# Optimization experiments

Hardware: AMD Instinct MI355X
Metric: run time of the kernel (lower is better)

Reference implementation:

```python
import jax, jax.numpy as jnp
import numpy as np

B, P, E, F = 65536, 16, 32, 64  # batch, n_patches, n_edges, feature_dim


def setup_inputs() -> dict:
    key = jax.random.key(0)
    k1, k2 = jax.random.split(key, 2)
    node_sections = jax.random.normal(k1, (B, P, F), dtype=jnp.float32)
    incidence = (jax.random.normal(k2, (E, P), dtype=jnp.float32) * 0.1)
    # torch init: each sheaf map = eye(feature_dim) * 0.1, stacked -> [E, F, F]
    sheaf_maps = jnp.tile((jnp.eye(F, dtype=jnp.float32) * 0.1)[None], (E, 1, 1))
    damping = jnp.asarray(0.1, dtype=jnp.float32)
    return {"node_sections": node_sections, "incidence": incidence,
            "sheaf_maps": sheaf_maps, "damping": damping}


def reference(node_sections, incidence, sheaf_maps, damping):
    # Coboundary: weighted[b,e,:] = sum_p incidence[e,p] * sections[b,p,:];
    # then per-edge matmul with sheaf_maps[e].
    weighted = jnp.einsum('ep,bpf->bef', incidence, node_sections)
    coboundary = jnp.einsum('bef,efg->beg', weighted, sheaf_maps)
    # Laplacian diffusion: delta^T delta [P,P] applied over patch dim.
    dTd = jnp.einsum('ep,eq->pq', incidence, incidence)
    diffused = node_sections - damping * jnp.einsum('pq,bqf->bpf', dTd, node_sections)
    # H1 energy proxy: per-edge L2 norm, averaged over edges -> [B]
    h1_norm = jnp.linalg.norm(coboundary, axis=-1).mean(axis=-1)
    return diffused, h1_norm
```

## Files before the change

### kernel.cpp

```cpp
#include <hip/hip_runtime.h>
#include <hip/hip_bf16.h>

typedef __attribute__((ext_vector_type(8))) short short8;
typedef __attribute__((ext_vector_type(4))) float floatx4;

#define NB 65536
#define STS 18
#define WES 68
#define WBS 1092

static __device__ __forceinline__ ushort f2bf(float x) {
  union { float f; unsigned u; } v; v.f = x;
  unsigned r = v.u + 0x7FFFu + ((v.u >> 16) & 1u);
  return (ushort)(r >> 16);
}

__global__ void sheaf_prep(const float* __restrict__ inc,
                           const float* __restrict__ M,
                           const float* __restrict__ damp,
                           ushort* __restrict__ Mt,
                           ushort* __restrict__ L) {
  const int bid = blockIdx.x, tid = threadIdx.x;
  if (bid < 32) {
    const float* Me = M + (bid << 12);
    ushort* Mte = Mt + (bid << 12);
    for (int i = tid; i < 4096; i += 256) {
      int g = i >> 6, f = i & 63;
      Mte[(g << 6) + f] = f2bf(Me[(f << 6) + g]);
    }
  } else {
    for (int i = tid; i < 1024; i += 256) {
      int e = i >> 5, col = i & 31;
      L[(e << 5) + col] = (col < 16) ? f2bf(inc[(e << 4) + col]) : (ushort)0;
    }
    float d = damp[0];
    int p = tid >> 4, q = tid & 15;
    float s = 0.f;
    for (int e = 0; e < 32; ++e)
      s += inc[(e << 4) + p] * inc[(e << 4) + q];
    float a = ((p == q) ? 1.f : 0.f) - d * s;
    L[((32 + p) << 5) + q] = f2bf(a);
    L[((32 + p) << 5) + 16 + q] = (ushort)0;
  }
}

__global__ __launch_bounds__(256, 2) void sheaf_main(
    const float* __restrict__ S,
    const ushort* __restrict__ Mt,
    const ushort* __restrict__ L,
    float* __restrict__ out) {
  __shared__ ushort st[1024 * STS];
  __shared__ ushort wl[16 * WBS];
  __shared__ float h1s[4][16];

  const int tid = threadIdx.x;
  const int lane = tid & 63;
  const int w = tid >> 6;
  const int quad = lane >> 4;
  const int l15 = lane & 15;

  {
    const float4* gS = (const float4*)S + (size_t)blockIdx.x * 4096;
    #pragma unroll
    for (int i = 0; i < 16; ++i) {
      int v = tid + (i << 8);
      float4 raw = gS[v];
      int b = v >> 8, p = (v >> 4) & 15, fv = v & 15;
      int base = ((b << 6) + (fv << 2)) * STS + p;
      st[base]           = f2bf(raw.x);
      st[base + STS]     = f2bf(raw.y);
      st[base + 2 * STS] = f2bf(raw.z);
      st[base + 3 * STS] = f2bf(raw.w);
    }
  }

  short8 aL0 = *(const short8*)(L + (l15) * 32 + (quad << 3));
  short8 aL1 = *(const short8*)(L + (16 + l15) * 32 + (quad << 3));
  short8 aLp = *(const short8*)(L + (32 + l15) * 32 + (quad << 3));

  __syncthreads();

  float hp = 0.f;

  for (int ec = 0; ec < 2; ++ec) {
    short8 aE = ec ? aL1 : aL0;
    for (int t = 0; t < 16; ++t) {
      int ctile = (w << 4) + t;
      int c = (ctile << 4) + l15;
      short8 bf;
      {
        union { short8 v; unsigned wds[4]; } u;
        if (quad < 2) {
          const unsigned* row = (const unsigned*)(st + c * STS);
          int o = quad << 2;
          u.wds[0] = row[o];     u.wds[1] = row[o + 1];
          u.wds[2] = row[o + 2]; u.wds[3] = row[o + 3];
        } else {
          u.wds[0] = 0u; u.wds[1] = 0u; u.wds[2] = 0u; u.wds[3] = 0u;
        }
        bf = u.v;
      }
      floatx4 acc = {0.f, 0.f, 0.f, 0.f};
      acc = __builtin_amdgcn_mfma_f32_16x16x32_bf16(aE, bf, acc, 0, 0, 0);
      int b = c >> 6, f = c & 63;
      int wbase = b * WBS + f;
      #pragma unroll
      for (int r = 0; r < 4; ++r) {
        int eloc = (quad << 2) + r;
        wl[wbase + eloc * WES] = f2bf(acc[r]);
      }
      if (ec == 0) {
        floatx4 accD = {0.f, 0.f, 0.f, 0.f};
        accD = __builtin_amdgcn_mfma_f32_16x16x32_bf16(aLp, bf, accD, 0, 0, 0);
        size_t obase = ((size_t)blockIdx.x * 16 + (size_t)b) * 1024 + (size_t)f;
        #pragma unroll
        for (int r = 0; r < 4; ++r) {
          int p = (quad << 2) + r;
          out[obase + p * 64] = accD[r];
        }
      }
    }
    __syncthreads();

    #pragma unroll
    for (int i = 0; i < 4; ++i) {
      int eloc = (w << 2) + i;
      int e = (ec << 4) + eloc;
      const ushort* MtE = Mt + (e << 12);
      float ss = 0.f;
      #pragma unroll
      for (int gt = 0; gt < 4; ++gt) {
        floatx4 acc = {0.f, 0.f, 0.f, 0.f};
        #pragma unroll
        for (int ks = 0; ks < 2; ++ks) {
          short8 af = *(const short8*)(MtE + (((gt << 4) + l15) << 6) + (ks << 5) + (quad << 3));
          union { short8 v; uint2 u2[2]; } ub;
          const uint2* pw = (const uint2*)(wl + l15 * WBS + eloc * WES + (ks << 5) + (quad << 3));
          ub.u2[0] = pw[0]; ub.u2[1] = pw[1];
          acc = __builtin_amdgcn_mfma_f32_16x16x32_bf16(af, ub.v, acc, 0, 0, 0);
        }
        ss += acc[0]*acc[0] + acc[1]*acc[1] + acc[2]*acc[2] + acc[3]*acc[3];
      }
      ss += __shfl_xor(ss, 16);
      ss += __shfl_xor(ss, 32);
      hp += sqrtf(ss);
    }
    __syncthreads();
  }

  if (lane < 16) h1s[w][l15] = hp;
  __syncthreads();
  if (tid < 16) {
    float tsum = (h1s[0][tid] + h1s[1][tid] + h1s[2][tid] + h1s[3][tid]) * (1.f / 32.f);
    out[(size_t)NB * 1024 + (size_t)blockIdx.x * 16 + tid] = tsum;
  }
}

extern "C" void kernel_launch(void* const* d_in, const int* in_sizes, int n_in,
                              void* d_out, int out_size, void* d_ws, size_t ws_size,
                              hipStream_t stream) {
  const float* S   = (const float*)d_in[0];
  const float* inc = (const float*)d_in[1];
  const float* M   = (const float*)d_in[2];
  const float* dmp = (const float*)d_in[3];
  float* out = (float*)d_out;

  ushort* Mt = (ushort*)d_ws;
  ushort* L  = Mt + 131072;

  sheaf_prep<<<33, 256, 0, stream>>>(inc, M, dmp, Mt, L);
  sheaf_main<<<NB / 16, 256, 0, stream>>>(S, Mt, L, out);
}
```

Measured before the change: 526.3 us.

## Load sections directly into MFMA operands, drop staging LDS, raise occupancy

Each lane now reads the fp32 node sections straight from global memory and packs them into bf16 MFMA A-operands, so the shared staging buffer and its transpose are gone. Both edge-half coboundary products and the diffusion product are computed in a single pass, and the second half's results are held in registers until the first half's sheaf-map stage has run. Diffused outputs are written as float4 and weighted values as packed uint2, and launch bounds go from 2 to 4 blocks per CU because less LDS is used. The trade-off is strided, less coalesced global loads and extra register pressure from the 16-entry stash.

```diff
diff --git a/kernel.cpp b/kernel.cpp
--- a/kernel.cpp
+++ b/kernel.cpp
@@ -1,18 +1,20 @@
 #include <hip/hip_runtime.h>
-#include <hip/hip_bf16.h>
 
 typedef __attribute__((ext_vector_type(8))) short short8;
 typedef __attribute__((ext_vector_type(4))) float floatx4;
 
 #define NB 65536
-#define STS 18
-#define WES 68
-#define WBS 1092
+#define WES 72
+#define WBS 1160
 
 static __device__ __forceinline__ ushort f2bf(float x) {
   union { float f; unsigned u; } v; v.f = x;
   unsigned r = v.u + 0x7FFFu + ((v.u >> 16) & 1u);
   return (ushort)(r >> 16);
+}
+
+static __device__ __forceinline__ unsigned pk2(float lo, float hi) {
+  return (unsigned)f2bf(lo) | ((unsigned)f2bf(hi) << 16);
 }
 
 __global__ void sheaf_prep(const float* __restrict__ inc,
@@ -44,13 +46,12 @@
   }
 }
 
-__global__ __launch_bounds__(256, 2) void sheaf_main(
+__global__ __launch_bounds__(256, 4) void sheaf_main(
     const float* __restrict__ S,
     const ushort* __restrict__ Mt,
     const ushort* __restrict__ L,
     float* __restrict__ out) {
-  __shared__ ushort st[1024 * STS];
-  __shared__ ushort wl[16 * WBS];
+  __shared__ __align__(16) ushort wl[16 * WBS];
   __shared__ float h1s[4][16];
 
   const int tid = threadIdx.x;
@@ -58,75 +59,48 @@
   const int w = tid >> 6;
   const int quad = lane >> 4;
   const int l15 = lane & 15;
+  const int h = quad & 1;
 
-  {
-    const float4* gS = (const float4*)S + (size_t)blockIdx.x * 4096;
-    #pragma unroll
-    for (int i = 0; i < 16; ++i) {
-      int v = tid + (i << 8);
-      float4 raw = gS[v];
-      int b = v >> 8, p = (v >> 4) & 15, fv = v & 15;
-      int base = ((b << 6) + (fv << 2)) * STS + p;
-      st[base]           = f2bf(raw.x);
-      st[base + STS]     = f2bf(raw.y);
-      st[base + 2 * STS] = f2bf(raw.z);
-      st[base + 3 * STS] = f2bf(raw.w);
-    }
+  short8 bL0 = *(const short8*)(L + (l15) * 32 + (quad << 3));
+  short8 bL1 = *(const short8*)(L + (16 + l15) * 32 + (quad << 3));
+  short8 bLp = *(const short8*)(L + (32 + l15) * 32 + (quad << 3));
+
+  float hp = 0.f;
+  uint2 stash[16];
+
+  #pragma unroll
+  for (int t = 0; t < 16; ++t) {
+    const int ctile = (w << 4) + t;
+    const int b = ctile >> 2;
+    const int f0 = ((t & 3) << 4) + (quad << 2);
+    const float* gp = S + ((((size_t)blockIdx.x << 4) + b) << 10)
+                        + (h << 9) + ((t & 3) << 4) + l15;
+    float g0 = gp[0],   g1 = gp[64],  g2 = gp[128], g3 = gp[192];
+    float g4 = gp[256], g5 = gp[320], g6 = gp[384], g7 = gp[448];
+    union { short8 v; unsigned u[4]; } fa;
+    fa.u[0] = pk2(g0, g1); fa.u[1] = pk2(g2, g3);
+    fa.u[2] = pk2(g4, g5); fa.u[3] = pk2(g6, g7);
+
+    floatx4 a0 = {0.f, 0.f, 0.f, 0.f};
+    floatx4 a1 = {0.f, 0.f, 0.f, 0.f};
+    floatx4 aD = {0.f, 0.f, 0.f, 0.f};
+    a0 = __builtin_amdgcn_mfma_f32_16x16x32_bf16(fa.v, bL0, a0, 0, 0, 0);
+    a1 = __builtin_amdgcn_mfma_f32_16x16x32_bf16(fa.v, bL1, a1, 0, 0, 0);
+    aD = __builtin_amdgcn_mfma_f32_16x16x32_bf16(fa.v, bLp, aD, 0, 0, 0);
+
+    uint2 wv; wv.x = pk2(a0[0], a0[1]); wv.y = pk2(a0[2], a0[3]);
+    *(uint2*)(wl + b * WBS + l15 * WES + f0) = wv;
+    uint2 sv; sv.x = pk2(a1[0], a1[1]); sv.y = pk2(a1[2], a1[3]);
+    stash[t] = sv;
+    float4 dv = make_float4(aD[0], aD[1], aD[2], aD[3]);
+    *(float4*)(out + ((((size_t)blockIdx.x << 4) + b) << 10) + (l15 << 6) + f0) = dv;
   }
 
-  short8 aL0 = *(const short8*)(L + (l15) * 32 + (quad << 3));
-  short8 aL1 = *(const short8*)(L + (16 + l15) * 32 + (quad << 3));
-  short8 aLp = *(const short8*)(L + (32 + l15) * 32 + (quad << 3));
-
-  __syncthreads();
-
-  float hp = 0.f;
-
-  for (int ec = 0; ec < 2; ++ec) {
-    short8 aE = ec ? aL1 : aL0;
-    for (int t = 0; t < 16; ++t) {
-      int ctile = (w << 4) + t;
-      int c = (ctile << 4) + l15;
-      short8 bf;
-      {
-        union { short8 v; unsigned wds[4]; } u;
-        if (quad < 2) {
-          const unsigned* row = (const unsigned*)(st + c * STS);
-          int o = quad << 2;
-          u.wds[0] = row[o];     u.wds[1] = row[o + 1];
-          u.wds[2] = row[o + 2]; u.wds[3] = row[o + 3];
-        } else {
-          u.wds[0] = 0u; u.wds[1] = 0u; u.wds[2] = 0u; u.wds[3] = 0u;
-        }
-        bf = u.v;
-      }
-      floatx4 acc = {0.f, 0.f, 0.f, 0.f};
-      acc = __builtin_amdgcn_mfma_f32_16x16x32_bf16(aE, bf, acc, 0, 0, 0);
-      int b = c >> 6, f = c & 63;
-      int wbase = b * WBS + f;
-      #pragma unroll
-      for (int r = 0; r < 4; ++r) {
-        int eloc = (quad << 2) + r;
-        wl[wbase + eloc * WES] = f2bf(acc[r]);
-      }
-      if (ec == 0) {
-        floatx4 accD = {0.f, 0.f, 0.f, 0.f};
-        accD = __builtin_amdgcn_mfma_f32_16x16x32_bf16(aLp, bf, accD, 0, 0, 0);
-        size_t obase = ((size_t)blockIdx.x * 16 + (size_t)b) * 1024 + (size_t)f;
-        #pragma unroll
-        for (int r = 0; r < 4; ++r) {
-          int p = (quad << 2) + r;
-          out[obase + p * 64] = accD[r];
-        }
-      }
-    }
-    __syncthreads();
-
+  auto step2 = [&](int ec) {
     #pragma unroll
     for (int i = 0; i < 4; ++i) {
-      int eloc = (w << 2) + i;
-      int e = (ec << 4) + eloc;
-      const ushort* MtE = Mt + (e << 12);
+      const int eloc = (w << 2) + i;
+      const ushort* MtE = Mt + (((ec << 4) + eloc) << 12);
       float ss = 0.f;
       #pragma unroll
       for (int gt = 0; gt < 4; ++gt) {
@@ -145,8 +119,20 @@
       ss += __shfl_xor(ss, 32);
       hp += sqrtf(ss);
     }
-    __syncthreads();
+  };
+
+  __syncthreads();
+  step2(0);
+  __syncthreads();
+
+  #pragma unroll
+  for (int t = 0; t < 16; ++t) {
+    const int b = ((w << 4) + t) >> 2;
+    const int f0 = ((t & 3) << 4) + (quad << 2);
+    *(uint2*)(wl + b * WBS + l15 * WES + f0) = stash[t];
   }
+  __syncthreads();
+  step2(1);
 
   if (lane < 16) h1s[w][l15] = hp;
   __syncthreads();
```

New measurement: 569.3 us. 1.08x slower.
